# Kernel optimization log

Measured on AMD Instinct MI355X. Metric: run time of the kernel, lower is better.

## Reference

```python
import jax, jax.numpy as jnp
import numpy as np

M_FILT = 16      # number of dendrite filters m
CLASSES = 10
IMG = 96         # input image side
N = 9            # dendrite window side
B = 16           # batch
S = IMG - N + 1  # 88, sliding-window output side
SP = S // 4      # 22, after MaxPool3d((4,4,1))


def setup_inputs() -> dict:
    key = jax.random.key(0)
    ks = jax.random.split(key, 7)
    x = jax.random.normal(ks[0], (B, IMG, IMG), jnp.float32)
    w = jax.random.normal(ks[1], (M_FILT, N, N), jnp.float32)
    q = jax.random.normal(ks[2], (M_FILT, N, N), jnp.float32)
    fin = M_FILT * SP * SP
    fc1_w = jax.random.normal(ks[3], (128, fin), jnp.float32) / np.sqrt(fin).astype(np.float32)
    fc1_b = jax.random.normal(ks[4], (128,), jnp.float32) * 0.01
    fc2_w = jax.random.normal(ks[5], (CLASSES, 128), jnp.float32) / np.float32(np.sqrt(128.0))
    fc2_b = jax.random.normal(ks[6], (CLASSES,), jnp.float32) * 0.01
    return dict(x=x, w=w, q=q, fc1_w=fc1_w, fc1_b=fc1_b, fc2_w=fc2_w, fc2_b=fc2_b)


def _dendrite(x, w, q):
    # Faithful to torch: y = (pi + 2*atan(10*(x*w - q))) / (2*pi);
    # prod over window cols (dim 5), log, sum over window rows (dim 4).
    # Computed window-offset-by-window-offset to avoid materializing
    # the [B,S,S,m,N,N] tensor the torch code builds.
    b = x.shape[0]
    acc = jnp.zeros((b, S, S, M_FILT), x.dtype)
    for r in range(N):
        rowprod = jnp.ones((b, S, S, M_FILT), x.dtype)
        for c in range(N):
            xs = x[:, r:r + S, c:c + S][..., None]          # [B,S,S,1]
            t = (jnp.pi + 2.0 * jnp.arctan(10.0 * (xs * w[:, r, c] - q[:, r, c]))) / (2.0 * jnp.pi)
            rowprod = rowprod * (t + 0.6)                   # prod over cols
        acc = acc + jnp.log(rowprod)                        # log then sum over rows
    return acc  # [B,S,S,M_FILT]


def reference(x, w, q, fc1_w, fc1_b, fc2_w, fc2_b):
    y = _dendrite(x, w, q)                                  # [B,S,S,m]
    b = y.shape[0]
    # Soma: MaxPool3d((4,4,1)) over (S,S,m) dims (stride = kernel)
    y = y.reshape(b, SP, 4, SP, 4, M_FILT).max(axis=(2, 4))  # [B,SP,SP,m]
    # Axon: flatten + Linear(fin,128) + ReLU  (torch view keeps memory order)
    y = y.reshape(b, M_FILT * SP * SP)
    h = jnp.maximum(y @ fc1_w.T + fc1_b, 0.0)               # [B,128]
    # Synapse: Linear(128, classes)
    return h @ fc2_w.T + fc2_b                              # [B,classes]
```

## Files before the change

kernel.cpp:

```cpp
#include <hip/hip_runtime.h>

#define BATCH 16
#define IMG 96
#define NWIN 9
#define M_FILT 16
#define SP 22
#define FIN (M_FILT * SP * SP)
#define NPP (SP * SP)

typedef float f32x2 __attribute__((ext_vector_type(2)));
typedef float f32x4 __attribute__((ext_vector_type(4)));

__device__ __forceinline__ f32x2 pk_mul(f32x2 a, f32x2 b) {
    f32x2 d;
    asm("v_pk_mul_f32 %0, %1, %2" : "=v"(d) : "v"(a), "v"(b));
    return d;
}
__device__ __forceinline__ f32x2 pk_fma(f32x2 a, f32x2 b, f32x2 c) {
    f32x2 d;
    asm("v_pk_fma_f32 %0, %1, %2, %3" : "=v"(d) : "v"(a), "v"(b), "v"(c));
    return d;
}

__device__ __forceinline__ f32x2 dend_t2(f32x2 z, f32x2 CK0, f32x2 CK1,
                                         f32x2 CK2, f32x2 CK3, f32x2 CK4) {
    float rx = __builtin_amdgcn_rcpf(z.x);
    float ry = __builtin_amdgcn_rcpf(z.y);
    bool bx = __builtin_fabsf(z.x) > 1.0f;
    bool by = __builtin_fabsf(z.y) > 1.0f;
    f32x2 u;
    u.x = bx ? -rx : z.x;
    u.y = by ? -ry : z.y;
    f32x2 s = pk_mul(u, u);
    f32x2 p = pk_fma(s, CK4, CK3);
    p = pk_fma(s, p, CK2);
    p = pk_fma(s, p, CK1);
    p = pk_fma(s, p, CK0);
    f32x2 c;
    float sgx = __builtin_copysignf(0.5f, z.x);
    float sgy = __builtin_copysignf(0.5f, z.y);
    c.x = 1.1f + (bx ? sgx : 0.0f);
    c.y = 1.1f + (by ? sgy : 0.0f);
    return pk_fma(u, p, c);
}

__global__ __launch_bounds__(256) void dendrite_pool_kernel(
    const float* __restrict__ x,
    const float* __restrict__ w,
    const float* __restrict__ q,
    float* __restrict__ pooled)
{
    const int tid   = threadIdx.x;
    const int chunk = blockIdx.x & 7;
    const int m     = (blockIdx.x >> 3) & 15;
    const int b     = blockIdx.x >> 7;

    __shared__ f32x2 swq[NWIN * NWIN];
    if (tid < NWIN * NWIN) {
        float wv = w[m * 81 + tid];
        float qv = q[m * 81 + tid];
        f32x2 t; t.x = 10.0f * wv; t.y = -10.0f * qv;
        swq[tid] = t;
    }
    __syncthreads();

    const int di  = tid & 3;
    const int ppl = tid >> 2;
    const int pp  = chunk * 64 + ppl;
    const int ppc = pp < NPP ? pp : (NPP - 1);
    const int pj  = ppc % SP;
    const int pi  = ppc / SP;

    const float* xb = x + b * IMG * IMG + (pi * 4 + di) * IMG + pj * 4;

    const f32x2 CK0 = { 0.3183026482f,  0.3183026482f};
    const f32x2 CK1 = {-0.10587727f,   -0.10587727f};
    const f32x2 CK2 = { 0.06160671f,    0.06160671f};
    const f32x2 CK3 = {-0.03706178f,   -0.03706178f};
    const f32x2 CK4 = { 0.01676006f,    0.01676006f};

    f32x2 PA = {1.0f, 1.0f};
    f32x2 PB = {1.0f, 1.0f};

    #pragma unroll 1
    for (int r = 0; r < NWIN; ++r) {
        const f32x4* xr = reinterpret_cast<const f32x4*>(xb + r * IMG);
        f32x4 X0 = xr[0], X1 = xr[1], X2 = xr[2];
        float xv[12] = {X0.x,X0.y,X0.z,X0.w, X1.x,X1.y,X1.z,X1.w, X2.x,X2.y,X2.z,X2.w};

        #pragma unroll
        for (int c = 0; c < 9; ++c) {
            f32x2 wq = swq[r * 9 + c];
            f32x2 zA, zB;
            zA.x = fmaf(xv[c + 0], wq.x, wq.y);
            zA.y = fmaf(xv[c + 1], wq.x, wq.y);
            zB.x = fmaf(xv[c + 2], wq.x, wq.y);
            zB.y = fmaf(xv[c + 3], wq.x, wq.y);
            PA = pk_mul(PA, dend_t2(zA, CK0, CK1, CK2, CK3, CK4));
            PB = pk_mul(PB, dend_t2(zB, CK0, CK1, CK2, CK3, CK4));
        }
    }

    float best = fmaxf(fmaxf(PA.x, PA.y), fmaxf(PB.x, PB.y));
    best = fmaxf(best, __shfl_xor(best, 1, 64));
    best = fmaxf(best, __shfl_xor(best, 2, 64));
    if (di == 0 && pp < NPP) {
        pooled[b * FIN + pp * 16 + m] = __builtin_amdgcn_logf(best) * 0.69314718056f;
    }
}

__global__ __launch_bounds__(256) void fc1_kernel(
    const float* __restrict__ pooled,
    const float* __restrict__ w1,
    const float* __restrict__ b1,
    float* __restrict__ h)
{
    int o = blockIdx.x;
    const float* wr = w1 + o * FIN;

    float acc[BATCH];
    #pragma unroll
    for (int b = 0; b < BATCH; ++b) acc[b] = 0.f;

    for (int f = threadIdx.x; f < FIN; f += 256) {
        float wv = wr[f];
        #pragma unroll
        for (int b = 0; b < BATCH; ++b)
            acc[b] = fmaf(pooled[b * FIN + f], wv, acc[b]);
    }

    #pragma unroll
    for (int b = 0; b < BATCH; ++b) {
        #pragma unroll
        for (int off = 32; off > 0; off >>= 1)
            acc[b] += __shfl_down(acc[b], off, 64);
    }

    __shared__ float red[4][BATCH];
    int wid = threadIdx.x >> 6, lane = threadIdx.x & 63;
    if (lane == 0) {
        #pragma unroll
        for (int b = 0; b < BATCH; ++b) red[wid][b] = acc[b];
    }
    __syncthreads();
    if (threadIdx.x < BATCH) {
        int b = threadIdx.x;
        float s_ = red[0][b] + red[1][b] + red[2][b] + red[3][b] + b1[o];
        h[b * 128 + o] = fmaxf(s_, 0.f);
    }
}

__global__ __launch_bounds__(192) void fc2_kernel(
    const float* __restrict__ h,
    const float* __restrict__ w2,
    const float* __restrict__ b2,
    float* __restrict__ out)
{
    int t = threadIdx.x;
    if (t >= BATCH * 10) return;
    int b = t / 10;
    int c = t - b * 10;
    const float* hb = h + b * 128;
    const float* wr = w2 + c * 128;
    float s = 0.0f;
    #pragma unroll 8
    for (int k = 0; k < 128; ++k) s += hb[k] * wr[k];
    out[t] = s + b2[c];
}

extern "C" void kernel_launch(void* const* d_in, const int* in_sizes, int n_in,
                              void* d_out, int out_size, void* d_ws, size_t ws_size,
                              hipStream_t stream)
{
    const float* x    = (const float*)d_in[0];
    const float* w    = (const float*)d_in[1];
    const float* q    = (const float*)d_in[2];
    const float* fc1w = (const float*)d_in[3];
    const float* fc1b = (const float*)d_in[4];
    const float* fc2w = (const float*)d_in[5];
    const float* fc2b = (const float*)d_in[6];
    float* out = (float*)d_out;

    float* pooled = (float*)d_ws;
    float* h      = pooled + BATCH * FIN;

    dendrite_pool_kernel<<<2048, 256, 0, stream>>>(x, w, q, pooled);
    fc1_kernel<<<128, 256, 0, stream>>>(pooled, fc1w, fc1b, h);
    fc2_kernel<<<1, 192, 0, stream>>>(h, fc2w, fc2b, out);
}
```

Before: 141.3 us.

## Lower arctan polynomial degree, branchless offset, fuse fc2 into fc1 via atomics

Shortens the arctan minimax polynomial from five to three coefficients and computes the branch offset with trunc plus med3 clamp. This cuts VALU work in the dendrite inner loop. It also fuses the fc2 layer into the fc1 kernel: each output-neuron block atomically adds its contribution into the logits, which the dendrite kernel pre-initialises with the fc2 bias. The fc1 block size goes from 256 to 512 threads, removing one launch. The lower-degree polynomial lowers arctan accuracy, and the atomics make the result order nondeterministic.

```diff
diff --git a/kernel.cpp b/kernel.cpp
--- a/kernel.cpp
+++ b/kernel.cpp
@@ -22,8 +22,7 @@
     return d;
 }
 
-__device__ __forceinline__ f32x2 dend_t2(f32x2 z, f32x2 CK0, f32x2 CK1,
-                                         f32x2 CK2, f32x2 CK3, f32x2 CK4) {
+__device__ __forceinline__ f32x2 dend_t2(f32x2 z, f32x2 CK0, f32x2 CK1, f32x2 CK2) {
     float rx = __builtin_amdgcn_rcpf(z.x);
     float ry = __builtin_amdgcn_rcpf(z.y);
     bool bx = __builtin_fabsf(z.x) > 1.0f;
@@ -32,15 +31,11 @@
     u.x = bx ? -rx : z.x;
     u.y = by ? -ry : z.y;
     f32x2 s = pk_mul(u, u);
-    f32x2 p = pk_fma(s, CK4, CK3);
-    p = pk_fma(s, p, CK2);
-    p = pk_fma(s, p, CK1);
+    f32x2 p = pk_fma(s, CK2, CK1);
     p = pk_fma(s, p, CK0);
     f32x2 c;
-    float sgx = __builtin_copysignf(0.5f, z.x);
-    float sgy = __builtin_copysignf(0.5f, z.y);
-    c.x = 1.1f + (bx ? sgx : 0.0f);
-    c.y = 1.1f + (by ? sgy : 0.0f);
+    c.x = fmaf(__builtin_amdgcn_fmed3f(truncf(z.x), -1.0f, 1.0f), 0.5f, 1.1f);
+    c.y = fmaf(__builtin_amdgcn_fmed3f(truncf(z.y), -1.0f, 1.0f), 0.5f, 1.1f);
     return pk_fma(u, p, c);
 }
 
@@ -48,12 +43,18 @@
     const float* __restrict__ x,
     const float* __restrict__ w,
     const float* __restrict__ q,
-    float* __restrict__ pooled)
+    float* __restrict__ pooled,
+    const float* __restrict__ fc2b,
+    float* __restrict__ out)
 {
     const int tid   = threadIdx.x;
     const int chunk = blockIdx.x & 7;
     const int m     = (blockIdx.x >> 3) & 15;
     const int b     = blockIdx.x >> 7;
+
+    if (blockIdx.x == 0 && tid < BATCH * 10) {
+        out[tid] = fc2b[tid % 10];
+    }
 
     __shared__ f32x2 swq[NWIN * NWIN];
     if (tid < NWIN * NWIN) {
@@ -73,11 +74,9 @@
 
     const float* xb = x + b * IMG * IMG + (pi * 4 + di) * IMG + pj * 4;
 
-    const f32x2 CK0 = { 0.3183026482f,  0.3183026482f};
-    const f32x2 CK1 = {-0.10587727f,   -0.10587727f};
-    const f32x2 CK2 = { 0.06160671f,    0.06160671f};
-    const f32x2 CK3 = {-0.03706178f,   -0.03706178f};
-    const f32x2 CK4 = { 0.01676006f,    0.01676006f};
+    const f32x2 CK0 = { 0.3167024f,  0.3167024f};
+    const f32x2 CK1 = {-0.0907569f, -0.0907569f};
+    const f32x2 CK2 = { 0.0240536f,  0.0240536f};
 
     f32x2 PA = {1.0f, 1.0f};
     f32x2 PB = {1.0f, 1.0f};
@@ -86,18 +85,20 @@
     for (int r = 0; r < NWIN; ++r) {
         const f32x4* xr = reinterpret_cast<const f32x4*>(xb + r * IMG);
         f32x4 X0 = xr[0], X1 = xr[1], X2 = xr[2];
-        float xv[12] = {X0.x,X0.y,X0.z,X0.w, X1.x,X1.y,X1.z,X1.w, X2.x,X2.y,X2.z,X2.w};
+        float xs[12] = {X0.x, X0.y, X0.z, X0.w,
+                        X1.x, X1.y, X1.z, X1.w,
+                        X2.x, X2.y, X2.z, X2.w};
 
         #pragma unroll
         for (int c = 0; c < 9; ++c) {
             f32x2 wq = swq[r * 9 + c];
             f32x2 zA, zB;
-            zA.x = fmaf(xv[c + 0], wq.x, wq.y);
-            zA.y = fmaf(xv[c + 1], wq.x, wq.y);
-            zB.x = fmaf(xv[c + 2], wq.x, wq.y);
-            zB.y = fmaf(xv[c + 3], wq.x, wq.y);
-            PA = pk_mul(PA, dend_t2(zA, CK0, CK1, CK2, CK3, CK4));
-            PB = pk_mul(PB, dend_t2(zB, CK0, CK1, CK2, CK3, CK4));
+            zA.x = fmaf(xs[c + 0], wq.x, wq.y);
+            zA.y = fmaf(xs[c + 1], wq.x, wq.y);
+            zB.x = fmaf(xs[c + 2], wq.x, wq.y);
+            zB.y = fmaf(xs[c + 3], wq.x, wq.y);
+            PA = pk_mul(PA, dend_t2(zA, CK0, CK1, CK2));
+            PB = pk_mul(PB, dend_t2(zB, CK0, CK1, CK2));
         }
     }
 
@@ -109,11 +110,12 @@
     }
 }
 
-__global__ __launch_bounds__(256) void fc1_kernel(
+__global__ __launch_bounds__(512) void fc_fused_kernel(
     const float* __restrict__ pooled,
     const float* __restrict__ w1,
     const float* __restrict__ b1,
-    float* __restrict__ h)
+    const float* __restrict__ w2,
+    float* __restrict__ out)
 {
     int o = blockIdx.x;
     const float* wr = w1 + o * FIN;
@@ -122,7 +124,7 @@
     #pragma unroll
     for (int b = 0; b < BATCH; ++b) acc[b] = 0.f;
 
-    for (int f = threadIdx.x; f < FIN; f += 256) {
+    for (int f = threadIdx.x; f < FIN; f += 512) {
         float wv = wr[f];
         #pragma unroll
         for (int b = 0; b < BATCH; ++b)
@@ -136,7 +138,8 @@
             acc[b] += __shfl_down(acc[b], off, 64);
     }
 
-    __shared__ float red[4][BATCH];
+    __shared__ float red[8][BATCH];
+    __shared__ float hrow[BATCH];
     int wid = threadIdx.x >> 6, lane = threadIdx.x & 63;
     if (lane == 0) {
         #pragma unroll
@@ -145,27 +148,16 @@
     __syncthreads();
     if (threadIdx.x < BATCH) {
         int b = threadIdx.x;
-        float s_ = red[0][b] + red[1][b] + red[2][b] + red[3][b] + b1[o];
-        h[b * 128 + o] = fmaxf(s_, 0.f);
+        float s_ = b1[o];
+        #pragma unroll
+        for (int k = 0; k < 8; ++k) s_ += red[k][b];
+        hrow[b] = fmaxf(s_, 0.f);
     }
-}
-
-__global__ __launch_bounds__(192) void fc2_kernel(
-    const float* __restrict__ h,
-    const float* __restrict__ w2,
-    const float* __restrict__ b2,
-    float* __restrict__ out)
-{
-    int t = threadIdx.x;
-    if (t >= BATCH * 10) return;
-    int b = t / 10;
-    int c = t - b * 10;
-    const float* hb = h + b * 128;
-    const float* wr = w2 + c * 128;
-    float s = 0.0f;
-    #pragma unroll 8
-    for (int k = 0; k < 128; ++k) s += hb[k] * wr[k];
-    out[t] = s + b2[c];
+    __syncthreads();
+    if (threadIdx.x < BATCH * 10) {
+        int b = threadIdx.x / 10, c = threadIdx.x % 10;
+        atomicAdd(&out[b * 10 + c], hrow[b] * w2[c * 128 + o]);
+    }
 }
 
 extern "C" void kernel_launch(void* const* d_in, const int* in_sizes, int n_in,
@@ -182,9 +174,7 @@
     float* out = (float*)d_out;
 
     float* pooled = (float*)d_ws;
-    float* h      = pooled + BATCH * FIN;
 
-    dendrite_pool_kernel<<<2048, 256, 0, stream>>>(x, w, q, pooled);
-    fc1_kernel<<<128, 256, 0, stream>>>(pooled, fc1w, fc1b, h);
-    fc2_kernel<<<1, 192, 0, stream>>>(h, fc2w, fc2b, out);
+    dendrite_pool_kernel<<<2048, 256, 0, stream>>>(x, w, q, pooled, fc2b, out);
+    fc_fused_kernel<<<128, 512, 0, stream>>>(pooled, fc1w, fc1b, fc2w, out);
 }
```

Result: faster. 128.7 us (-8.9%).
